# Kernel tuning notes

Hardware: AMD Instinct MI355X
Metric: run time of the kernel (lower is better)

The kernel has to match this reference:

```python
import jax, jax.numpy as jnp
import numpy as np

GROUP = 64  # group_size from module


def setup_inputs() -> dict:
    key = jax.random.key(0)
    ks = jax.random.split(key, 7)
    B, S, N, K = 4, 2048, 4096, 4096  # in_features=N, out_features=K
    G = N // GROUP
    x = jax.random.normal(ks[0], (B, S, N), dtype=jnp.float32)
    W_q = jax.random.randint(ks[1], (K, N), 0, 16, dtype=jnp.int32)  # 4-bit codes
    scales = jax.random.uniform(ks[2], (K, G), dtype=jnp.float32, minval=0.01, maxval=1.0)
    zeros = jax.random.uniform(ks[3], (K, G), dtype=jnp.float32, minval=0.0, maxval=15.0)
    mask = jax.random.randint(ks[4], (K, N), 0, 2, dtype=jnp.int32)  # unstructured sparsity mask
    scale2 = jax.random.uniform(ks[5], (K, 1), dtype=jnp.float32, minval=0.5, maxval=1.5)
    bias = jax.random.normal(ks[6], (K,), dtype=jnp.float32)
    return {"x": x, "W_q": W_q, "scales": scales, "zeros": zeros,
            "mask": mask, "scale2": scale2, "bias": bias}


def _dequantize_sparse_sinq(W_q, scales, zeros, mask, scale2, dtype):
    # W_q: (K, N) int codes; scales/zeros: (K, N//GROUP) per-(row,group);
    # scale2: (K, 1) second (Sinkhorn) row scale; mask: (K, N) sparsity mask.
    K, N = W_q.shape
    G = N // GROUP
    Wg = W_q.astype(dtype).reshape(K, G, GROUP)
    W = (Wg - zeros[:, :, None]) * scales[:, :, None]  # grouped affine dequant
    W = W.reshape(K, N) * scale2                       # dual-scale compensation
    W = W * mask.astype(dtype)                         # apply unstructured sparsity
    return W


def reference(x, W_q, scales, zeros, mask, scale2, bias):
    W = _dequantize_sparse_sinq(W_q, scales, zeros, mask, scale2, x.dtype)  # (K, N)
    out = jnp.einsum('bsn,kn->bsk', x, W) + bias  # x @ W.T + bias
    return out
```

## Files before the change

### kernel.cpp

```cpp
#include <hip/hip_runtime.h>


#define M_DIM 8192
#define N_DIM 4096
#define K_DIM 4096
#define NT 64

typedef __bf16 bf16;
typedef __attribute__((ext_vector_type(8))) bf16 bf16x8;
typedef __attribute__((ext_vector_type(4))) float f32x4;
typedef __attribute__((ext_vector_type(4))) float f32x4v;
typedef __attribute__((ext_vector_type(4))) int   i32x4v;

__global__ __launch_bounds__(256) void cvt_x_kernel(const float* __restrict__ x,
                                                    bf16* __restrict__ xb) {
  const long total = (long)M_DIM * N_DIM / 8;
  const long stride = (long)gridDim.x * blockDim.x;
  for (long t = (long)blockIdx.x * blockDim.x + threadIdx.x; t < total; t += stride) {
    const long e = t * 8;
    const f32x4v v0 = __builtin_nontemporal_load(reinterpret_cast<const f32x4v*>(x + e));
    const f32x4v v1 = __builtin_nontemporal_load(reinterpret_cast<const f32x4v*>(x + e + 4));
    bf16x8 o;
    o[0] = (bf16)v0[0]; o[1] = (bf16)v0[1]; o[2] = (bf16)v0[2]; o[3] = (bf16)v0[3];
    o[4] = (bf16)v1[0]; o[5] = (bf16)v1[1]; o[6] = (bf16)v1[2]; o[7] = (bf16)v1[3];
    *reinterpret_cast<bf16x8*>(xb + e) = o;
  }
}

__global__ __launch_bounds__(256) void deq_w_kernel(const int* __restrict__ Wq,
                                                    const float* __restrict__ scales,
                                                    const float* __restrict__ zeros,
                                                    const int* __restrict__ mask,
                                                    const float* __restrict__ scale2,
                                                    bf16* __restrict__ wb) {
  const int total = K_DIM * (N_DIM / 8);
  const int stride = gridDim.x * blockDim.x;
  for (int t = blockIdx.x * blockDim.x + threadIdx.x; t < total; t += stride) {
    const int k = t >> 9;
    const int n0 = (t & 511) << 3;
    const int g = n0 >> 6;
    const float s = scales[(k << 6) + g] * scale2[k];
    const float z = zeros[(k << 6) + g];
    const long base = (long)k * N_DIM + n0;
    const i32x4v q0 = __builtin_nontemporal_load(reinterpret_cast<const i32x4v*>(Wq + base));
    const i32x4v q1 = __builtin_nontemporal_load(reinterpret_cast<const i32x4v*>(Wq + base + 4));
    const i32x4v m0 = __builtin_nontemporal_load(reinterpret_cast<const i32x4v*>(mask + base));
    const i32x4v m1 = __builtin_nontemporal_load(reinterpret_cast<const i32x4v*>(mask + base + 4));
    bf16x8 o;
    o[0] = (bf16)(((float)q0[0] - z) * s * (float)m0[0]);
    o[1] = (bf16)(((float)q0[1] - z) * s * (float)m0[1]);
    o[2] = (bf16)(((float)q0[2] - z) * s * (float)m0[2]);
    o[3] = (bf16)(((float)q0[3] - z) * s * (float)m0[3]);
    o[4] = (bf16)(((float)q1[0] - z) * s * (float)m1[0]);
    o[5] = (bf16)(((float)q1[1] - z) * s * (float)m1[1]);
    o[6] = (bf16)(((float)q1[2] - z) * s * (float)m1[2]);
    o[7] = (bf16)(((float)q1[3] - z) * s * (float)m1[3]);
    *reinterpret_cast<bf16x8*>(wb + base) = o;
  }
}

__device__ inline void gload16(const bf16* g, bf16* l) {
  __builtin_amdgcn_global_load_lds(
      (const __attribute__((address_space(1))) void*)g,
      (__attribute__((address_space(3))) void*)l, 16, 0, 0);
}

#define BARRIER asm volatile("s_barrier" ::: "memory")
#define LGKM0   asm volatile("s_waitcnt lgkmcnt(0)" ::: "memory")
#define VM6     asm volatile("s_waitcnt vmcnt(6)" ::: "memory")
#define VM0     asm volatile("s_waitcnt vmcnt(0)" ::: "memory")
#define SBAR    __builtin_amdgcn_sched_barrier(0)

__global__ __launch_bounds__(512, 2) void gemm_kernel(const bf16* __restrict__ xb,
                                                      const bf16* __restrict__ wb,
                                                      const float* __restrict__ bias,
                                                      float* __restrict__ out) {
  __shared__ bf16 lds[65536];

  const int tid = threadIdx.x;
  const int lane = tid & 63;
  const int w = tid >> 6;
  const int wr = w >> 2;
  const int wc = w & 3;

  const int gid = blockIdx.x;
  const int idx = gid >> 3;
  const int bm = (gid & 7) * 4 + (idx >> 4);
  const int bk = idx & 15;
  const long m0 = (long)bm * 256;
  const long k0 = (long)bk * 256;

  const int browA = tid >> 3;
  const int slotA = (tid & 7) ^ (browA & 7);
  const bf16* baseA = xb + (m0 + browA) * N_DIM + slotA * 8;
  const int u = tid & 255;
  const int wcb = tid >> 8;
  const int browB = u >> 3;
  const int slotB = (u & 7) ^ (browB & 7);
  const bf16* baseB = wb + (k0 + wcb * 64 + browB) * N_DIM + slotB * 8;

  const int ln15 = lane & 15;
  const int x0 = (lane >> 4) ^ (lane & 7);
  int aoffk[2], boffk[2];
#pragma unroll
  for (int kk = 0; kk < 2; ++kk) {
    const int x = x0 ^ (kk << 2);
    aoffk[kk] = (wr * 128 + ln15) * 64 + x * 8;
    boffk[kk] = 16384 + (wc * 64 + ln15) * 64 + x * 8;
  }

  f32x4 acc[8][4] = {};
  bf16x8 afH0[4][2], afH1[4][2], bfA[2][2], bfB[2][2];

  auto STA = [&](int tt, int bsel, int h) {
    const bf16* s = baseA + (long)(h * 64) * N_DIM + tt * 64;
    bf16* d = lds + bsel * 32768 + h * 4096 + (tid << 3);
    gload16(s, d);
    gload16(s + (long)128 * N_DIM, d + 8192);
  };
  auto STB = [&](int tt, int bsel, int h) {
    const bf16* s = baseB + (long)(h * 32) * N_DIM + tt * 64;
    bf16* d = lds + bsel * 32768 + 16384 + wcb * 4096 + h * 2048 + (u << 3);
    gload16(s, d);
    gload16(s + (long)128 * N_DIM, d + 8192);
  };
  auto LDA = [&](bf16x8 (*dst)[2], int cb, int mh) {
#pragma unroll
    for (int mf = 0; mf < 4; ++mf)
#pragma unroll
      for (int kk = 0; kk < 2; ++kk)
        dst[mf][kk] = *reinterpret_cast<const bf16x8*>(
            lds + cb + aoffk[kk] + mh * 4096 + mf * 1024);
  };
  auto LDB = [&](bf16x8 (*dst)[2], int cb, int nh) {
#pragma unroll
    for (int nf = 0; nf < 2; ++nf)
#pragma unroll
      for (int kk = 0; kk < 2; ++kk)
        dst[nf][kk] = *reinterpret_cast<const bf16x8*>(
            lds + cb + boffk[kk] + nh * 2048 + nf * 1024);
  };
  auto MFMA_Q = [&](bf16x8 (*a4)[2], bf16x8 (*bf)[2], int mh, int nh) {
#pragma unroll
    for (int kk = 0; kk < 2; ++kk)
#pragma unroll
      for (int mf = 0; mf < 4; ++mf)
#pragma unroll
        for (int nf = 0; nf < 2; ++nf)
          acc[mh * 4 + mf][nh * 2 + nf] = __builtin_amdgcn_mfma_f32_16x16x32_bf16(
              a4[mf][kk], bf[nf][kk], acc[mh * 4 + mf][nh * 2 + nf], 0, 0, 0);
  };

  STA(0, 0, 0); STB(0, 0, 0); STB(0, 0, 1); STA(0, 0, 1);
  STA(1, 1, 0); STB(1, 1, 0); STB(1, 1, 1);
  VM6; BARRIER;
  LDA(afH0, 0, 0); LDB(bfA, 0, 0);

  auto TILE = [&](int t, int c) {
    const int cb = c * 32768;
    const int ob = (c ^ 1) * 32768;
    if (t + 1 < NT) STA(t + 1, c ^ 1, 1);
    BARRIER; LGKM0; SBAR;
    __builtin_amdgcn_s_setprio(1);
    LDB(bfB, cb, 1);
    MFMA_Q(afH0, bfA, 0, 0);
    __builtin_amdgcn_s_setprio(0);
    BARRIER; LGKM0; SBAR;
    __builtin_amdgcn_s_setprio(1);
    LDA(afH1, cb, 1);
    MFMA_Q(afH0, bfB, 0, 1);
    __builtin_amdgcn_s_setprio(0);
    if (t + 2 < NT) { STA(t + 2, c, 0); STB(t + 2, c, 0); }
    BARRIER; LGKM0; SBAR;
    __builtin_amdgcn_s_setprio(1);
    MFMA_Q(afH1, bfA, 1, 0);
    __builtin_amdgcn_s_setprio(0);
    if (t + 2 < NT) STB(t + 2, c, 1);
    if (t < NT - 2) { VM6; } else { VM0; }
    BARRIER; LGKM0; SBAR;
    __builtin_amdgcn_s_setprio(1);
    if (t + 1 < NT) { LDA(afH0, ob, 0); LDB(bfA, ob, 0); }
    MFMA_Q(afH1, bfB, 1, 1);
    __builtin_amdgcn_s_setprio(0);
  };

  for (int tp = 0; tp < NT / 2; ++tp) {
    TILE(2 * tp, 0);
    TILE(2 * tp + 1, 1);
  }

  const int ocol0 = (int)k0 + wc * 64 + ln15;
  const int orow0 = (int)m0 + wr * 128 + (lane >> 4) * 4;
#pragma unroll
  for (int ni = 0; ni < 4; ++ni) {
    const float bv = bias[ocol0 + ni * 16];
#pragma unroll
    for (int mi = 0; mi < 8; ++mi)
#pragma unroll
      for (int r = 0; r < 4; ++r)
        __builtin_nontemporal_store(
            acc[mi][ni][r] + bv,
            &out[(long)(orow0 + mi * 16 + r) * K_DIM + ocol0 + ni * 16]);
  }
}

extern "C" void kernel_launch(void* const* d_in, const int* in_sizes, int n_in,
                              void* d_out, int out_size, void* d_ws, size_t ws_size,
                              hipStream_t stream) {
  const float* x      = (const float*)d_in[0];
  const int*   Wq     = (const int*)d_in[1];
  const float* scales = (const float*)d_in[2];
  const float* zeros  = (const float*)d_in[3];
  const int*   mask   = (const int*)d_in[4];
  const float* scale2 = (const float*)d_in[5];
  const float* bias   = (const float*)d_in[6];
  float* out = (float*)d_out;

  bf16* xb = (bf16*)d_ws;
  bf16* wb = (bf16*)((char*)d_ws + (size_t)M_DIM * N_DIM * 2);

  cvt_x_kernel<<<2048, 256, 0, stream>>>(x, xb);
  deq_w_kernel<<<2048, 256, 0, stream>>>(Wq, scales, zeros, mask, scale2, wb);

  gemm_kernel<<<512, 512, 0, stream>>>(xb, wb, bias, out);
}
```

Baseline: 282.4 us.

## Restructure GEMM main loop into two barrier phases per K-tile

Reworks the GEMM inner pipeline from four barrier-separated quarter phases to two phases per K-tile. B fragments for both halves are loaded together, and next-tile LDS reads are interleaved with the last MFMA quarters. The vmcnt waits are retuned to match the new issue order. The goal is fewer s_barrier stalls and better overlap of LDS reads with MFMA, at the cost of more live registers and a riskier wait/hazard schedule. The loop is also no longer manually unrolled by two, so the buffer selector becomes a runtime value.

```diff
diff --git a/kernel.cpp b/kernel.cpp
--- a/kernel.cpp
+++ b/kernel.cpp
@@ -67,7 +67,9 @@
 
 #define BARRIER asm volatile("s_barrier" ::: "memory")
 #define LGKM0   asm volatile("s_waitcnt lgkmcnt(0)" ::: "memory")
+#define VM8     asm volatile("s_waitcnt vmcnt(8)" ::: "memory")
 #define VM6     asm volatile("s_waitcnt vmcnt(6)" ::: "memory")
+#define VM2     asm volatile("s_waitcnt vmcnt(2)" ::: "memory")
 #define VM0     asm volatile("s_waitcnt vmcnt(0)" ::: "memory")
 #define SBAR    __builtin_amdgcn_sched_barrier(0)
 
@@ -132,13 +134,11 @@
         dst[mf][kk] = *reinterpret_cast<const bf16x8*>(
             lds + cb + aoffk[kk] + mh * 4096 + mf * 1024);
   };
-  auto LDB = [&](bf16x8 (*dst)[2], int cb, int nh) {
-#pragma unroll
-    for (int nf = 0; nf < 2; ++nf)
-#pragma unroll
-      for (int kk = 0; kk < 2; ++kk)
-        dst[nf][kk] = *reinterpret_cast<const bf16x8*>(
-            lds + cb + boffk[kk] + nh * 2048 + nf * 1024);
+  auto LDB1 = [&](bf16x8* dst, int cb, int nh, int nf) {
+#pragma unroll
+    for (int kk = 0; kk < 2; ++kk)
+      dst[kk] = *reinterpret_cast<const bf16x8*>(
+          lds + cb + boffk[kk] + nh * 2048 + nf * 1024);
   };
   auto MFMA_Q = [&](bf16x8 (*a4)[2], bf16x8 (*bf)[2], int mh, int nh) {
 #pragma unroll
@@ -154,39 +154,33 @@
   STA(0, 0, 0); STB(0, 0, 0); STB(0, 0, 1); STA(0, 0, 1);
   STA(1, 1, 0); STB(1, 1, 0); STB(1, 1, 1);
   VM6; BARRIER;
-  LDA(afH0, 0, 0); LDB(bfA, 0, 0);
-
-  auto TILE = [&](int t, int c) {
+  LDA(afH0, 0, 0);
+  LDB1(bfA[0], 0, 0, 0); LDB1(bfA[1], 0, 0, 1);
+  LDB1(bfB[0], 0, 1, 0); LDB1(bfB[1], 0, 1, 1);
+
+  for (int s = 0; s < NT; ++s) {
+    const int c = s & 1;
     const int cb = c * 32768;
     const int ob = (c ^ 1) * 32768;
-    if (t + 1 < NT) STA(t + 1, c ^ 1, 1);
-    BARRIER; LGKM0; SBAR;
-    __builtin_amdgcn_s_setprio(1);
-    LDB(bfB, cb, 1);
-    MFMA_Q(afH0, bfA, 0, 0);
-    __builtin_amdgcn_s_setprio(0);
-    BARRIER; LGKM0; SBAR;
+    if (s + 1 < NT) { STA(s + 1, c ^ 1, 1); VM8; } else { VM0; }
+    LGKM0;
+    BARRIER; SBAR;
     __builtin_amdgcn_s_setprio(1);
     LDA(afH1, cb, 1);
+    MFMA_Q(afH0, bfA, 0, 0);
     MFMA_Q(afH0, bfB, 0, 1);
     __builtin_amdgcn_s_setprio(0);
-    if (t + 2 < NT) { STA(t + 2, c, 0); STB(t + 2, c, 0); }
-    BARRIER; LGKM0; SBAR;
+    if (s + 2 < NT) { STA(s + 2, c, 0); STB(s + 2, c, 0); STB(s + 2, c, 1); VM8; }
+    else if (s + 1 < NT) { VM2; }
+    LGKM0;
+    BARRIER; SBAR;
     __builtin_amdgcn_s_setprio(1);
+    if (s + 1 < NT) LDA(afH0, ob, 0);
     MFMA_Q(afH1, bfA, 1, 0);
+    if (s + 1 < NT) { LDB1(bfA[0], ob, 0, 0); LDB1(bfA[1], ob, 0, 1); }
+    MFMA_Q(afH1, bfB, 1, 1);
+    if (s + 1 < NT) { LDB1(bfB[0], ob, 1, 0); LDB1(bfB[1], ob, 1, 1); }
     __builtin_amdgcn_s_setprio(0);
-    if (t + 2 < NT) STB(t + 2, c, 1);
-    if (t < NT - 2) { VM6; } else { VM0; }
-    BARRIER; LGKM0; SBAR;
-    __builtin_amdgcn_s_setprio(1);
-    if (t + 1 < NT) { LDA(afH0, ob, 0); LDB(bfA, ob, 0); }
-    MFMA_Q(afH1, bfB, 1, 1);
-    __builtin_amdgcn_s_setprio(0);
-  };
-
-  for (int tp = 0; tp < NT / 2; ++tp) {
-    TILE(2 * tp, 0);
-    TILE(2 * tp + 1, 1);
   }
 
   const int ocol0 = (int)k0 + wc * 64 + ln15;
```

New measurement: 279.4 us. About the same (-1.1%).
